# Performance work log

Measured on AMD Instinct MI355X. Metric: run time of the kernel, lower is better.

The kernel has to match this reference:

```python
import jax, jax.numpy as jnp
import numpy as np

N_ITER = 30  # bisection iterations for entmax-1.5 threshold


def segment_entmax15(x, seg, num_segments):
    """Entmax alpha=1.5 over variable-size segments (the DGL mailbox dim).
    p_i = [ (alpha-1)*x_i - tau ]_+ ** (1/(alpha-1)), sum_segment p = 1.
    Threshold tau found by bisection per segment (monotone decreasing sum).
    """
    X = 0.5 * x  # (alpha-1) * x
    m = jax.ops.segment_max(X, seg, num_segments=num_segments)

    def body(i, bounds):
        lo, hi = bounds
        tau = 0.5 * (lo + hi)
        p = jnp.square(jnp.maximum(X - tau[seg], 0.0))
        s = jax.ops.segment_sum(p, seg, num_segments=num_segments)
        lo = jnp.where(s > 1.0, tau, lo)
        hi = jnp.where(s > 1.0, hi, tau)
        return (lo, hi)

    lo, hi = jax.lax.fori_loop(0, N_ITER, body, (m - 1.0, m))
    tau = 0.5 * (lo + hi)
    p = jnp.square(jnp.maximum(X - tau[seg], 0.0))
    denom = jax.ops.segment_sum(p, seg, num_segments=num_segments)
    return p / jnp.maximum(denom, 1e-12)[seg]


def setup_inputs() -> dict:
    key = jax.random.key(0)
    k1, k2, k3, k4, k5, k6 = jax.random.split(key, 6)
    N, E = 100000, 3200000
    in_dim, out_dim, num_community = 128, 64, 32
    h = jax.random.normal(k1, (N, in_dim), dtype=jnp.float32)
    u = jax.random.normal(k2, (N, num_community), dtype=jnp.float32)
    src = jax.random.randint(k3, (E,), 0, N, dtype=jnp.int32)
    dst = jax.random.randint(k4, (E,), 0, N, dtype=jnp.int32)
    Wfc = jax.random.normal(k5, (out_dim, in_dim), dtype=jnp.float32) * (1.0 / np.sqrt(in_dim))
    W2 = jax.random.normal(k6, (1, 2 * num_community), dtype=jnp.float32) * (1.0 / np.sqrt(2 * num_community))
    return {"h": h, "u": u, "src": src, "dst": dst, "Wfc": Wfc, "W2": W2}


def reference(h, u, src, dst, Wfc, W2):
    N = h.shape[0]
    # node transform: z = fc(h)
    z = h @ Wfc.T  # [N, out_dim]
    # edge attention: a = attn_fc2(cat(u_src, u_dst)); entmax over dim=1 of
    # a [E,1] tensor is over a singleton axis -> identically 1.0
    z2 = jnp.concatenate([u[src], u[dst]], axis=1)  # [E, 2*num_community]
    a = z2 @ W2.T  # [E, 1]
    e = jnp.ones_like(a)[:, 0]  # entmax-1.5 over singleton dim == 1
    # reduce: alpha = entmax15 over each destination node's mailbox of e
    alpha = segment_entmax15(e, dst, N)  # [E]
    # h_v = sum_{e->v} alpha_e * z_src(e) * e_e
    contrib = (alpha * e)[:, None] * z[src]  # [E, out_dim]
    h_out = jax.ops.segment_sum(contrib, dst, num_segments=N)
    return h_out
```

## Files before the change

kernel.cpp:

```cpp
#include <hip/hip_runtime.h>
#include <hip/hip_fp16.h>


#define WS_ALIGN(x) (((x) + (size_t)255) & ~(size_t)255)
#define BBITS 6
#define BNODES 64
#define CAP 4096
#define MAXBUCK 2048

__device__ inline unsigned pack_h2(float a, float b) {
    __half2 h = __floats2half2_rn(a, b);
    return *reinterpret_cast<unsigned*>(&h);
}

__global__ __launch_bounds__(256) void bucket_count(const int* __restrict__ dst,
                                                    int* __restrict__ bcnt,
                                                    int E, int nbuck) {
    __shared__ int h[MAXBUCK];
    for (int i = threadIdx.x; i < nbuck; i += 256) h[i] = 0;
    __syncthreads();
    int base = blockIdx.x * 16384;
    for (int k = 0; k < 64; k++) {
        int e = base + threadIdx.x + k * 256;
        if (e < E) atomicAdd(&h[dst[e] >> BBITS], 1);
    }
    __syncthreads();
    for (int i = threadIdx.x; i < nbuck; i += 256)
        if (h[i]) atomicAdd(&bcnt[i], h[i]);
}

__global__ __launch_bounds__(1024) void scan_buckets(const int* __restrict__ bcnt,
                                                     int* __restrict__ bases,
                                                     int* __restrict__ cur,
                                                     int E, int nbuck) {
    __shared__ int sp[1024];
    int t = threadIdx.x;
    int a = (2 * t < nbuck) ? bcnt[2 * t] : 0;
    int b = (2 * t + 1 < nbuck) ? bcnt[2 * t + 1] : 0;
    sp[t] = a + b;
    __syncthreads();
    for (int off = 1; off < 1024; off <<= 1) {
        int x = (t >= off) ? sp[t - off] : 0;
        __syncthreads();
        sp[t] += x;
        __syncthreads();
    }
    int ex = sp[t] - (a + b);
    if (2 * t < nbuck)     { bases[2 * t] = ex;         cur[2 * t] = ex; }
    if (2 * t + 1 < nbuck) { bases[2 * t + 1] = ex + a; cur[2 * t + 1] = ex + a; }
    if (t == 0) bases[nbuck] = E;
}

__global__ __launch_bounds__(256) void bin_scatter(const int* __restrict__ src,
                                                   const int* __restrict__ dst,
                                                   int* __restrict__ cur,
                                                   unsigned* __restrict__ binned,
                                                   int E, int nbuck) {
    __shared__ int hist[MAXBUCK], gbase[MAXBUCK], cnt2[MAXBUCK];
    int base = blockIdx.x * 16384;
    for (int i = threadIdx.x; i < nbuck; i += 256) { hist[i] = 0; cnt2[i] = 0; }
    __syncthreads();
    for (int k = 0; k < 64; k++) {
        int e = base + threadIdx.x + k * 256;
        if (e < E) atomicAdd(&hist[dst[e] >> BBITS], 1);
    }
    __syncthreads();
    for (int i = threadIdx.x; i < nbuck; i += 256)
        if (hist[i]) gbase[i] = atomicAdd(&cur[i], hist[i]);
    __syncthreads();
    for (int k = 0; k < 64; k++) {
        int e = base + threadIdx.x + k * 256;
        if (e < E) {
            int d = dst[e];
            int b = d >> BBITS;
            int lo = atomicAdd(&cnt2[b], 1);
            binned[gbase[b] + lo] = ((unsigned)(d & (BNODES - 1)) << 17) |
                                    (unsigned)src[e];
        }
    }
}

__global__ __launch_bounds__(256) void gemm_z(const float* __restrict__ h,
                                              const float* __restrict__ W,
                                              __half* __restrict__ z, int N) {
    __shared__ float Wl[64 * 128];
    for (int j = threadIdx.x; j < 2048; j += 256) {
        reinterpret_cast<float4*>(Wl)[j] = reinterpret_cast<const float4*>(W)[j];
    }
    __syncthreads();
    int row = blockIdx.x * 256 + threadIdx.x;
    if (row >= N) return;
    float acc[64];
#pragma unroll
    for (int c = 0; c < 64; c++) acc[c] = 0.f;
    const float4* hr = reinterpret_cast<const float4*>(&h[(size_t)row * 128]);
    for (int kv = 0; kv < 32; kv++) {
        float4 hv = hr[kv];
#pragma unroll
        for (int c = 0; c < 64; c++) {
            float4 wv = *reinterpret_cast<const float4*>(&Wl[c * 128 + kv * 4]);
            acc[c] += hv.x * wv.x + hv.y * wv.y + hv.z * wv.z + hv.w * wv.w;
        }
    }
    uint4* zr = reinterpret_cast<uint4*>(&z[(size_t)row * 64]);
#pragma unroll
    for (int c = 0; c < 8; c++) {
        uint4 pk;
        pk.x = pack_h2(acc[8 * c + 0], acc[8 * c + 1]);
        pk.y = pack_h2(acc[8 * c + 2], acc[8 * c + 3]);
        pk.z = pack_h2(acc[8 * c + 4], acc[8 * c + 5]);
        pk.w = pack_h2(acc[8 * c + 6], acc[8 * c + 7]);
        zr[c] = pk;
    }
}

__global__ __launch_bounds__(256) void bucket_gather(
        const unsigned* __restrict__ binned,
        const int* __restrict__ bases,
        const __half* __restrict__ z,
        float* __restrict__ out, int N) {
    __shared__ unsigned sed[CAP];
    __shared__ int hist[BNODES];
    __shared__ int ioff[BNODES];
    __shared__ int eoff[BNODES];
    __shared__ int curs[BNODES];
    __shared__ int degl[BNODES];

    int b = blockIdx.x;
    int s0 = bases[b], s1 = bases[b + 1];
    int tid = threadIdx.x;
    int wid = tid >> 6, lane = tid & 63;

    if (tid < BNODES) degl[tid] = 0;

    float acc[16];
#pragma unroll
    for (int s = 0; s < 16; s++) acc[s] = 0.f;

    for (int c0 = s0; c0 < s1; c0 += CAP) {
        int cnt = s1 - c0;
        if (cnt > CAP) cnt = CAP;
        if (tid < BNODES) hist[tid] = 0;
        __syncthreads();
        for (int i = tid; i < cnt; i += 256) {
            unsigned p = binned[c0 + i];
            atomicAdd(&hist[(p >> 17) & (BNODES - 1)], 1);
        }
        __syncthreads();
        if (tid < BNODES) ioff[tid] = hist[tid];
        __syncthreads();
        for (int off = 1; off < BNODES; off <<= 1) {
            int x = 0;
            if (tid < BNODES && tid >= off) x = ioff[tid - off];
            __syncthreads();
            if (tid < BNODES) ioff[tid] += x;
            __syncthreads();
        }
        if (tid < BNODES) {
            int ex = ioff[tid] - hist[tid];
            eoff[tid] = ex;
            curs[tid] = ex;
            degl[tid] += hist[tid];
        }
        __syncthreads();
        for (int i = tid; i < cnt; i += 256) {
            unsigned p = binned[c0 + i];
            int ld = (p >> 17) & (BNODES - 1);
            int pos = atomicAdd(&curs[ld], 1);
            sed[pos] = p & 0x1FFFFu;
        }
        __syncthreads();
#pragma unroll
        for (int s = 0; s < 16; s++) {
            int r = wid * 16 + s;
            int e0 = eoff[r], e1 = ioff[r];
            float f0 = 0.f, f1 = 0.f, f2 = 0.f, f3 = 0.f;
            int e = e0;
            for (; e + 4 <= e1; e += 4) {
                int q0 = sed[e], q1 = sed[e + 1], q2 = sed[e + 2], q3 = sed[e + 3];
                f0 += __half2float(z[(size_t)q0 * 64 + lane]);
                f1 += __half2float(z[(size_t)q1 * 64 + lane]);
                f2 += __half2float(z[(size_t)q2 * 64 + lane]);
                f3 += __half2float(z[(size_t)q3 * 64 + lane]);
            }
            for (; e < e1; e++)
                f0 += __half2float(z[(size_t)sed[e] * 64 + lane]);
            acc[s] += (f0 + f1) + (f2 + f3);
        }
        __syncthreads();
    }
    int node0 = b << BBITS;
#pragma unroll
    for (int s = 0; s < 16; s++) {
        int node = node0 + wid * 16 + s;
        if (node < N) {
            int d = degl[wid * 16 + s];
            float sc = (d > 0) ? 1.0f / (float)d : 0.f;
            out[(size_t)node * 64 + lane] = acc[s] * sc;
        }
    }
}

__global__ __launch_bounds__(256) void count_deg(const int* __restrict__ dst,
                                                 int* __restrict__ cnt, int E) {
    int e = blockIdx.x * 256 + threadIdx.x;
    if (e < E) atomicAdd(&cnt[dst[e]], 1);
}

__global__ __launch_bounds__(256) void edge_add(const __half* __restrict__ z,
                                                const int* __restrict__ src,
                                                const int* __restrict__ dst,
                                                float* __restrict__ out, int E) {
    int e = blockIdx.x * 4 + (threadIdx.x >> 6);
    int lane = threadIdx.x & 63;
    if (e >= E) return;
    int s = src[e];
    int d = dst[e];
    float v = __half2float(z[(size_t)s * 64 + lane]);
    atomicAdd(&out[(size_t)d * 64 + lane], v);
}

__global__ __launch_bounds__(256) void scale_out(float* __restrict__ out,
                                                 const int* __restrict__ deg, int N) {
    int v = blockIdx.x * 4 + (threadIdx.x >> 6);
    int lane = threadIdx.x & 63;
    if (v >= N) return;
    int d = deg[v];
    if (d > 0) out[(size_t)v * 64 + lane] *= (1.0f / (float)d);
}

extern "C" void kernel_launch(void* const* d_in, const int* in_sizes, int n_in,
                              void* d_out, int out_size, void* d_ws, size_t ws_size,
                              hipStream_t stream) {
    const float* h   = (const float*)d_in[0];
    const int*   src = (const int*)d_in[2];
    const int*   dst = (const int*)d_in[3];
    const float* Wfc = (const float*)d_in[4];
    float*       out = (float*)d_out;

    int N = in_sizes[0] / 128;
    int E = in_sizes[2];
    (void)n_in; (void)out_size;

    int nbuck = (N + BNODES - 1) >> BBITS;

    size_t sz_z    = WS_ALIGN((size_t)N * 64 * sizeof(__half));
    size_t sz_bin  = WS_ALIGN((size_t)E * sizeof(unsigned));
    size_t sz_bkt  = WS_ALIGN((size_t)(3 * MAXBUCK + 2) * sizeof(int));
    size_t need_fast = sz_z + sz_bin + sz_bkt;

    char*     ws     = (char*)d_ws;
    __half*   z      = (__half*)ws;
    unsigned* binned = (unsigned*)(ws + sz_z);
    int*      bcnt   = (int*)(ws + sz_z + sz_bin);
    int*      bases  = bcnt + MAXBUCK;
    int*      cur    = bases + MAXBUCK + 2;

    int nwgE = (E + 16383) / 16384;

    bool can_fast = (N <= (1 << 17)) && (nbuck <= MAXBUCK) &&
                    (ws_size >= need_fast);

    if (can_fast) {
        hipMemsetAsync(bcnt, 0, (size_t)nbuck * sizeof(int), stream);
        bucket_count<<<nwgE, 256, 0, stream>>>(dst, bcnt, E, nbuck);
        scan_buckets<<<1, 1024, 0, stream>>>(bcnt, bases, cur, E, nbuck);
        bin_scatter<<<nwgE, 256, 0, stream>>>(src, dst, cur, binned, E, nbuck);
        gemm_z<<<(N + 255) / 256, 256, 0, stream>>>(h, Wfc, z, N);
        bucket_gather<<<nbuck, 256, 0, stream>>>(binned, bases, z, out, N);
    } else if (ws_size >= sz_z + WS_ALIGN((size_t)N * sizeof(int))) {
        int* deg = (int*)(ws + sz_z);
        hipMemsetAsync(deg, 0, (size_t)N * sizeof(int), stream);
        hipMemsetAsync(out, 0, (size_t)N * 64 * sizeof(float), stream);
        count_deg<<<(E + 255) / 256, 256, 0, stream>>>(dst, deg, E);
        gemm_z<<<(N + 255) / 256, 256, 0, stream>>>(h, Wfc, z, N);
        edge_add<<<(E + 3) / 4, 256, 0, stream>>>(z, src, dst, out, E);
        scale_out<<<(N + 3) / 4, 256, 0, stream>>>(out, deg, N);
    }
}
```

Baseline: 311.9 us.

## Reuse per-block bucket histograms for deterministic scatter offsets, shuffle scan, deeper unroll

```diff
diff --git a/kernel.cpp b/kernel.cpp
--- a/kernel.cpp
+++ b/kernel.cpp
@@ -7,6 +7,7 @@
 #define BNODES 64
 #define CAP 4096
 #define MAXBUCK 2048
+#define TILE 16384
 
 __device__ inline unsigned pack_h2(float a, float b) {
     __half2 h = __floats2half2_rn(a, b);
@@ -15,23 +16,27 @@
 
 __global__ __launch_bounds__(256) void bucket_count(const int* __restrict__ dst,
                                                     int* __restrict__ bcnt,
+                                                    int* __restrict__ hists,
                                                     int E, int nbuck) {
     __shared__ int h[MAXBUCK];
     for (int i = threadIdx.x; i < nbuck; i += 256) h[i] = 0;
     __syncthreads();
-    int base = blockIdx.x * 16384;
-    for (int k = 0; k < 64; k++) {
+    int base = blockIdx.x * TILE;
+    for (int k = 0; k < TILE / 256; k++) {
         int e = base + threadIdx.x + k * 256;
         if (e < E) atomicAdd(&h[dst[e] >> BBITS], 1);
     }
     __syncthreads();
-    for (int i = threadIdx.x; i < nbuck; i += 256)
-        if (h[i]) atomicAdd(&bcnt[i], h[i]);
+    int* hrow = hists + (size_t)blockIdx.x * nbuck;
+    for (int i = threadIdx.x; i < nbuck; i += 256) {
+        int v = h[i];
+        hrow[i] = v;
+        if (v) atomicAdd(&bcnt[i], v);
+    }
 }
 
 __global__ __launch_bounds__(1024) void scan_buckets(const int* __restrict__ bcnt,
                                                      int* __restrict__ bases,
-                                                     int* __restrict__ cur,
                                                      int E, int nbuck) {
     __shared__ int sp[1024];
     int t = threadIdx.x;
@@ -46,29 +51,50 @@
         __syncthreads();
     }
     int ex = sp[t] - (a + b);
-    if (2 * t < nbuck)     { bases[2 * t] = ex;         cur[2 * t] = ex; }
-    if (2 * t + 1 < nbuck) { bases[2 * t + 1] = ex + a; cur[2 * t + 1] = ex + a; }
+    if (2 * t < nbuck)     bases[2 * t] = ex;
+    if (2 * t + 1 < nbuck) bases[2 * t + 1] = ex + a;
     if (t == 0) bases[nbuck] = E;
+}
+
+__global__ __launch_bounds__(256) void scan_hists(int* __restrict__ hists,
+                                                  const int* __restrict__ bases,
+                                                  int nblk, int nbuck) {
+    int b = blockIdx.x * 256 + threadIdx.x;
+    if (b >= nbuck) return;
+    int run = bases[b];
+    int k = 0;
+    for (; k + 4 <= nblk; k += 4) {
+        size_t i0 = (size_t)(k + 0) * nbuck + b;
+        size_t i1 = (size_t)(k + 1) * nbuck + b;
+        size_t i2 = (size_t)(k + 2) * nbuck + b;
+        size_t i3 = (size_t)(k + 3) * nbuck + b;
+        int v0 = hists[i0], v1 = hists[i1], v2 = hists[i2], v3 = hists[i3];
+        hists[i0] = run; run += v0;
+        hists[i1] = run; run += v1;
+        hists[i2] = run; run += v2;
+        hists[i3] = run; run += v3;
+    }
+    for (; k < nblk; k++) {
+        size_t i = (size_t)k * nbuck + b;
+        int v = hists[i];
+        hists[i] = run; run += v;
+    }
 }
 
 __global__ __launch_bounds__(256) void bin_scatter(const int* __restrict__ src,
                                                    const int* __restrict__ dst,
-                                                   int* __restrict__ cur,
+                                                   const int* __restrict__ hists,
                                                    unsigned* __restrict__ binned,
                                                    int E, int nbuck) {
-    __shared__ int hist[MAXBUCK], gbase[MAXBUCK], cnt2[MAXBUCK];
-    int base = blockIdx.x * 16384;
-    for (int i = threadIdx.x; i < nbuck; i += 256) { hist[i] = 0; cnt2[i] = 0; }
-    __syncthreads();
-    for (int k = 0; k < 64; k++) {
-        int e = base + threadIdx.x + k * 256;
-        if (e < E) atomicAdd(&hist[dst[e] >> BBITS], 1);
-    }
-    __syncthreads();
-    for (int i = threadIdx.x; i < nbuck; i += 256)
-        if (hist[i]) gbase[i] = atomicAdd(&cur[i], hist[i]);
-    __syncthreads();
-    for (int k = 0; k < 64; k++) {
+    __shared__ int gbase[MAXBUCK], cnt2[MAXBUCK];
+    const int* hrow = hists + (size_t)blockIdx.x * nbuck;
+    for (int i = threadIdx.x; i < nbuck; i += 256) {
+        gbase[i] = hrow[i];
+        cnt2[i] = 0;
+    }
+    __syncthreads();
+    int base = blockIdx.x * TILE;
+    for (int k = 0; k < TILE / 256; k++) {
         int e = base + threadIdx.x + k * 256;
         if (e < E) {
             int d = dst[e];
@@ -147,20 +173,18 @@
             atomicAdd(&hist[(p >> 17) & (BNODES - 1)], 1);
         }
         __syncthreads();
-        if (tid < BNODES) ioff[tid] = hist[tid];
-        __syncthreads();
-        for (int off = 1; off < BNODES; off <<= 1) {
-            int x = 0;
-            if (tid < BNODES && tid >= off) x = ioff[tid - off];
-            __syncthreads();
-            if (tid < BNODES) ioff[tid] += x;
-            __syncthreads();
-        }
-        if (tid < BNODES) {
-            int ex = ioff[tid] - hist[tid];
-            eoff[tid] = ex;
-            curs[tid] = ex;
-            degl[tid] += hist[tid];
+        if (tid < 64) {
+            int v = hist[tid];
+            int inc = v;
+#pragma unroll
+            for (int off = 1; off < 64; off <<= 1) {
+                int x = __shfl_up(inc, off);
+                if (tid >= off) inc += x;
+            }
+            ioff[tid] = inc;
+            eoff[tid] = inc - v;
+            curs[tid] = inc - v;
+            degl[tid] += v;
         }
         __syncthreads();
         for (int i = tid; i < cnt; i += 256) {
@@ -175,7 +199,20 @@
             int r = wid * 16 + s;
             int e0 = eoff[r], e1 = ioff[r];
             float f0 = 0.f, f1 = 0.f, f2 = 0.f, f3 = 0.f;
+            float f4 = 0.f, f5 = 0.f, f6 = 0.f, f7 = 0.f;
             int e = e0;
+            for (; e + 8 <= e1; e += 8) {
+                int q0 = sed[e],     q1 = sed[e + 1], q2 = sed[e + 2], q3 = sed[e + 3];
+                int q4 = sed[e + 4], q5 = sed[e + 5], q6 = sed[e + 6], q7 = sed[e + 7];
+                f0 += __half2float(z[(size_t)q0 * 64 + lane]);
+                f1 += __half2float(z[(size_t)q1 * 64 + lane]);
+                f2 += __half2float(z[(size_t)q2 * 64 + lane]);
+                f3 += __half2float(z[(size_t)q3 * 64 + lane]);
+                f4 += __half2float(z[(size_t)q4 * 64 + lane]);
+                f5 += __half2float(z[(size_t)q5 * 64 + lane]);
+                f6 += __half2float(z[(size_t)q6 * 64 + lane]);
+                f7 += __half2float(z[(size_t)q7 * 64 + lane]);
+            }
             for (; e + 4 <= e1; e += 4) {
                 int q0 = sed[e], q1 = sed[e + 1], q2 = sed[e + 2], q3 = sed[e + 3];
                 f0 += __half2float(z[(size_t)q0 * 64 + lane]);
@@ -185,7 +222,7 @@
             }
             for (; e < e1; e++)
                 f0 += __half2float(z[(size_t)sed[e] * 64 + lane]);
-            acc[s] += (f0 + f1) + (f2 + f3);
+            acc[s] += ((f0 + f1) + (f2 + f3)) + ((f4 + f5) + (f6 + f7));
         }
         __syncthreads();
     }
@@ -240,32 +277,35 @@
 
     int N = in_sizes[0] / 128;
     int E = in_sizes[2];
-    (void)n_in; (void)out_size;
+    (void)n_in;
 
     int nbuck = (N + BNODES - 1) >> BBITS;
+    int nwgE  = (E + TILE - 1) / TILE;
 
     size_t sz_z    = WS_ALIGN((size_t)N * 64 * sizeof(__half));
     size_t sz_bin  = WS_ALIGN((size_t)E * sizeof(unsigned));
-    size_t sz_bkt  = WS_ALIGN((size_t)(3 * MAXBUCK + 2) * sizeof(int));
+    size_t sz_bkt  = WS_ALIGN((size_t)(2 * MAXBUCK + 2) * sizeof(int));
     size_t need_fast = sz_z + sz_bin + sz_bkt;
+    size_t need_hists = (size_t)nwgE * nbuck * sizeof(int);
 
     char*     ws     = (char*)d_ws;
     __half*   z      = (__half*)ws;
     unsigned* binned = (unsigned*)(ws + sz_z);
     int*      bcnt   = (int*)(ws + sz_z + sz_bin);
     int*      bases  = bcnt + MAXBUCK;
-    int*      cur    = bases + MAXBUCK + 2;
-
-    int nwgE = (E + 16383) / 16384;
+
+    int* hists = (int*)d_out;
 
     bool can_fast = (N <= (1 << 17)) && (nbuck <= MAXBUCK) &&
-                    (ws_size >= need_fast);
+                    (ws_size >= need_fast) &&
+                    ((size_t)out_size * sizeof(float) >= need_hists);
 
     if (can_fast) {
         hipMemsetAsync(bcnt, 0, (size_t)nbuck * sizeof(int), stream);
-        bucket_count<<<nwgE, 256, 0, stream>>>(dst, bcnt, E, nbuck);
-        scan_buckets<<<1, 1024, 0, stream>>>(bcnt, bases, cur, E, nbuck);
-        bin_scatter<<<nwgE, 256, 0, stream>>>(src, dst, cur, binned, E, nbuck);
+        bucket_count<<<nwgE, 256, 0, stream>>>(dst, bcnt, hists, E, nbuck);
+        scan_buckets<<<1, 1024, 0, stream>>>(bcnt, bases, E, nbuck);
+        scan_hists<<<(nbuck + 255) / 256, 256, 0, stream>>>(hists, bases, nwgE, nbuck);
+        bin_scatter<<<nwgE, 256, 0, stream>>>(src, dst, hists, binned, E, nbuck);
         gemm_z<<<(N + 255) / 256, 256, 0, stream>>>(h, Wfc, z, N);
         bucket_gather<<<nbuck, 256, 0, stream>>>(binned, bases, z, out, N);
     } else if (ws_size >= sz_z + WS_ALIGN((size_t)N * sizeof(int))) {
```

Result: slower. 414.9 us (+33.0%).
